# Kernel tuning notes

Measured on AMD Instinct MI355X. Metric: run time of the kernel, lower is better.

## Reference

```python
import jax, jax.numpy as jnp
import numpy as np

B, S, D = 1, 2048, 2048        # batch, max_seq_len, hidden_dim_attention
G, HPG = 4, 8                   # n_head_groups, n_heads_per_group
H = G * HPG                     # 32 total heads
DK = D // G                     # 512, KV projection width
HD = D // H                     # 64, head dim
EPS = 1e-6


def _embed_position(x, pm):
    # x: [B, S, d]; pm: [2, 1, S, D] -> uses pm[i][:, :, :d]
    d = x.shape[-1]
    _x = jnp.concatenate([-x[:, :, d // 2:], x[:, :, :d // 2]], axis=-1)
    # Faithful to source: BOTH terms use the rotated _x (source quirk).
    return _x * pm[0][:, :, :d] + _x * pm[1][:, :, :d]


def setup_inputs() -> dict:
    key = jax.random.key(0)
    k0, k1, k2, k3, k4, k5 = jax.random.split(key, 6)
    sc = 1.0 / np.sqrt(D).astype(np.float32)
    x = jax.random.normal(k0, (B, S, D), jnp.float32)
    position_matrix = jax.random.uniform(k1, (2, 1, S, D), jnp.float32)
    Wq = jax.random.normal(k2, (D, D), jnp.float32) * sc
    Wk = jax.random.normal(k3, (DK, D), jnp.float32) * sc
    Wv = jax.random.normal(k4, (DK, D), jnp.float32) * sc
    Wo = jax.random.normal(k5, (D, D), jnp.float32) * sc
    return {"x": x, "position_matrix": position_matrix,
            "Wq": Wq, "Wk": Wk, "Wv": Wv, "Wo": Wo}


def reference(x, position_matrix, Wq, Wk, Wv, Wo):
    xq = x @ Wq.T                                  # [B,S,D]
    xk = x @ Wk.T                                  # [B,S,DK]
    xv = x @ Wv.T                                  # [B,S,DK]
    xq = _embed_position(xq, position_matrix)
    xk = _embed_position(xk, position_matrix)
    # GQA expansion: replicate the DK-wide KV across G groups, split into heads.
    xk4 = jnp.broadcast_to(xk[:, :, None, :], (B, S, G, DK)).reshape(B, S, H, HD).transpose(0, 2, 1, 3)
    xv4 = jnp.broadcast_to(xv[:, :, None, :], (B, S, G, DK)).reshape(B, S, H, HD).transpose(0, 2, 1, 3)
    xq4 = xq.reshape(B, S, H, HD).transpose(0, 2, 1, 3)   # [B,H,S,HD]
    score = jnp.einsum('bhsd,bhtd->bhst', xq4, xk4) / (np.sqrt(DK) + EPS)
    # Source adds a tiny positive value (1e-10) above the diagonal, not -inf.
    mask = jnp.triu(jnp.full((S, S), 1e-10, jnp.float32), 1)
    score = score + mask
    e = jnp.exp(score.astype(jnp.float32))
    scores = (e / (jnp.sum(e, axis=-1, keepdims=True) + 1.0)).astype(xq4.dtype)
    out = jnp.einsum('bhst,bhtd->bhsd', scores, xv4)      # [B,H,S,HD]
    out = out.transpose(0, 2, 1, 3).reshape(B, S, D)
    return out @ Wo.T
```

## Files before the change

kernel.cpp:

```cpp
#include <hip/hip_runtime.h>
#include <cmath>

typedef unsigned short u16;
typedef unsigned int u32;
typedef __bf16 bf16x8 __attribute__((ext_vector_type(8)));
typedef __bf16 bf16x4 __attribute__((ext_vector_type(4)));
typedef float f32x4 __attribute__((ext_vector_type(4)));

#define S_LEN 2048
#define D_MODEL 2048
#define DK_ 512
#define PM1_OFF 4194304
#define CEXP 0.06375872f

__device__ __forceinline__ u16 f2b(float f) {
  u32 u = __float_as_uint(f);
  return (u16)((u + 0x7fffu + ((u >> 16) & 1u)) >> 16);
}

__device__ __forceinline__ void gload_lds16(const void* gp, void* lp) {
  __builtin_amdgcn_global_load_lds(
      (const __attribute__((address_space(1))) void*)gp,
      (__attribute__((address_space(3))) void*)lp, 16, 0, 0);
}

__device__ __forceinline__ void vmcnt0_barrier() {
  asm volatile("s_waitcnt vmcnt(0)" ::: "memory");
  __builtin_amdgcn_s_barrier();
}

__global__ __launch_bounds__(256) void cast_all_kernel(
    const float* __restrict__ x, const float* __restrict__ wq,
    const float* __restrict__ wk, const float* __restrict__ wv,
    const float* __restrict__ wo,
    u16* __restrict__ xb, u16* __restrict__ wqb, u16* __restrict__ wkb,
    u16* __restrict__ wvb, u16* __restrict__ wob)
{
  long i4 = (long)blockIdx.x * 256 + threadIdx.x;
  const float* src; u16* dst; long off;
  if (i4 < 1048576)       { src = x;  dst = xb;  off = i4; }
  else if (i4 < 2097152)  { src = wq; dst = wqb; off = i4 - 1048576; }
  else if (i4 < 2359296)  { src = wk; dst = wkb; off = i4 - 2097152; }
  else if (i4 < 2621440)  { src = wv; dst = wvb; off = i4 - 2359296; }
  else                    { src = wo; dst = wob; off = i4 - 2621440; }
  float4 v = *(const float4*)(src + off * 4);
  ushort4 o;
  o.x = f2b(v.x); o.y = f2b(v.y); o.z = f2b(v.z); o.w = f2b(v.w);
  *(ushort4*)(dst + off * 4) = o;
}

template<int EPI>
__global__ __launch_bounds__(256) void gemm_bt(
    const u16* __restrict__ A, const u16* __restrict__ B,
    void* __restrict__ C0, void* __restrict__ C1, void* __restrict__ C2,
    int M, int N, int K, const float* __restrict__ pm)
{
  __shared__ u16 As[2][64 * 64];
  __shared__ u16 Bs[2][128 * 64];
  const int tid = threadIdx.x;
  const int lane = tid & 63, w = tid >> 6;
  const int wr = w >> 1, wc = w & 1;
  const int l15 = lane & 15, l4 = lane >> 4;

  const int nwg = gridDim.x * gridDim.y;
  const int orig = blockIdx.y * gridDim.x + blockIdx.x;
  const int lin2 = (orig & 7) * (nwg >> 3) + (orig >> 3);
  const int m0 = (lin2 & 31) * 64;
  const int n0 = (lin2 >> 5) * 128;

  const int srow = tid >> 3;
  const int scol = ((tid & 7) ^ (srow & 7)) << 3;
  const int swz = (l15 & 7) << 3;
  const int ldsoff = (tid >> 6) << 10;
  const u16* gA = A + (size_t)(m0 + srow) * K + scol;
  const u16* gB = B + (size_t)(n0 + srow) * K + scol;

  const f32x4 z4 = {0.f, 0.f, 0.f, 0.f};
  f32x4 acc[2][4];
#pragma unroll
  for (int i = 0; i < 2; ++i)
#pragma unroll
    for (int j = 0; j < 4; ++j) acc[i][j] = z4;

  {
    char* la = (char*)As[0] + ldsoff;
    char* lb = (char*)Bs[0] + ldsoff;
#pragma unroll
    for (int i = 0; i < 2; ++i) gload_lds16(gA + (size_t)(i * 32) * K, la + i * 4096);
#pragma unroll
    for (int i = 0; i < 4; ++i) gload_lds16(gB + (size_t)(i * 32) * K, lb + i * 4096);
  }
  vmcnt0_barrier();

  const int NT = K >> 6;
  int cur = 0;
  for (int t = 0; t < NT; ++t) {
    if (t + 1 < NT) {
      const int kt = (t + 1) << 6;
      char* la = (char*)As[cur ^ 1] + ldsoff;
      char* lb = (char*)Bs[cur ^ 1] + ldsoff;
#pragma unroll
      for (int i = 0; i < 2; ++i) gload_lds16(gA + (size_t)(i * 32) * K + kt, la + i * 4096);
#pragma unroll
      for (int i = 0; i < 4; ++i) gload_lds16(gB + (size_t)(i * 32) * K + kt, lb + i * 4096);
    }
    const u16* as = As[cur];
    const u16* bs = Bs[cur];
#pragma unroll
    for (int ks = 0; ks < 2; ++ks) {
      bf16x8 a[2], b[4];
#pragma unroll
      for (int mt = 0; mt < 2; ++mt)
        a[mt] = *(const bf16x8*)(&as[(wr * 32 + mt * 16 + l15) * 64 + ((ks * 32 + l4 * 8) ^ swz)]);
#pragma unroll
      for (int nt = 0; nt < 4; ++nt)
        b[nt] = *(const bf16x8*)(&bs[(wc * 64 + nt * 16 + l15) * 64 + ((ks * 32 + l4 * 8) ^ swz)]);
#pragma unroll
      for (int mt = 0; mt < 2; ++mt)
#pragma unroll
        for (int nt = 0; nt < 4; ++nt)
          acc[mt][nt] = __builtin_amdgcn_mfma_f32_16x16x32_bf16(a[mt], b[nt], acc[mt][nt], 0, 0, 0);
    }
    vmcnt0_barrier();
    cur ^= 1;
  }

#pragma unroll
  for (int mt = 0; mt < 2; ++mt)
#pragma unroll
    for (int nt = 0; nt < 4; ++nt) {
      const int mb = m0 + wr * 32 + mt * 16 + l4 * 4;
      const int n = n0 + wc * 64 + nt * 16 + l15;
      if (EPI == 2) {
#pragma unroll
        for (int j = 0; j < 4; ++j)
          ((float*)C0)[(size_t)(mb + j) * N + n] = acc[mt][nt][j];
      } else if (n >= 2560) {
        const int c = n - 2560;
        ushort4 q;
        q.x = f2b(acc[mt][nt][0]); q.y = f2b(acc[mt][nt][1]);
        q.z = f2b(acc[mt][nt][2]); q.w = f2b(acc[mt][nt][3]);
        *(ushort4*)((u16*)C2 + (size_t)c * S_LEN + mb) = q;
      } else if (n < 2048) {
        const int jj = (n < 1024) ? (n + 1024) : (n - 1024);
#pragma unroll
        for (int j = 0; j < 4; ++j) {
          const int m = mb + j;
          const float sv = (n < 1024) ? acc[mt][nt][j] : -acc[mt][nt][j];
          const float p = pm[(size_t)m * D_MODEL + jj] +
                          pm[PM1_OFF + (size_t)m * D_MODEL + jj];
          ((u16*)C0)[(size_t)m * D_MODEL + jj] = f2b(sv * p * CEXP);
        }
      } else {
        const int nn = n - 2048;
        const int jj = (nn < 256) ? (nn + 256) : (nn - 256);
#pragma unroll
        for (int j = 0; j < 4; ++j) {
          const int m = mb + j;
          const float sv = (nn < 256) ? acc[mt][nt][j] : -acc[mt][nt][j];
          const float p = pm[(size_t)m * D_MODEL + jj] +
                          pm[PM1_OFF + (size_t)m * D_MODEL + jj];
          ((u16*)C1)[(size_t)m * DK_ + jj] = f2b(sv * p);
        }
      }
    }
}

__global__ __launch_bounds__(256) void attn_kernel(
    const u16* __restrict__ Q, const u16* __restrict__ Kx,
    const u16* __restrict__ Vt, u16* __restrict__ O)
{
  __shared__ u16 Ks[2][64 * 64];
  __shared__ u16 Vs[2][64 * 64];
  __shared__ u16 Es[4 * 32 * 64];

  const int tid = threadIdx.x;
  const int lane = tid & 63, w = tid >> 6;
  const int l15 = lane & 15, l4 = lane >> 4;

  const int orig = blockIdx.y * 16 + blockIdx.x;
  const int lin2 = (orig & 7) * 64 + (orig >> 3);
  const int h = lin2 >> 4;
  const int qb = lin2 & 15;
  const int q0 = qb * 128 + w * 32;
  const int hk = (h & 7) * 64;

  bf16x8 bq[2][2];
#pragma unroll
  for (int g = 0; g < 2; ++g)
#pragma unroll
    for (int ks = 0; ks < 2; ++ks)
      bq[g][ks] = *(const bf16x8*)(Q + (size_t)(q0 + g * 16 + l15) * D_MODEL
                                     + h * 64 + ks * 32 + l4 * 8);

  bf16x8 b1;
#pragma unroll
  for (int i = 0; i < 8; ++i) b1[i] = (__bf16)1.0f;

  const f32x4 z4 = {0.f, 0.f, 0.f, 0.f};
  f32x4 o[2][4], dsum[2];
#pragma unroll
  for (int g = 0; g < 2; ++g) {
    dsum[g] = z4;
#pragma unroll
    for (int nt = 0; nt < 4; ++nt) o[g][nt] = z4;
  }

  u16* Ew = Es + w * (32 * 64);
  const int swz = (l15 & 7) << 3;
  const int srow = tid >> 3;
  const int scol = ((tid & 7) ^ (srow & 7)) << 3;
  const int ldsoff = w << 10;
  const u16* gK = Kx + (size_t)srow * DK_ + hk + scol;
  const u16* gV = Vt + (size_t)(hk + srow) * S_LEN + scol;

  {
    char* lK = (char*)Ks[0] + ldsoff;
    char* lV = (char*)Vs[0] + ldsoff;
    gload_lds16(gK,                        lK);
    gload_lds16(gK + (size_t)32 * DK_,     lK + 4096);
    gload_lds16(gV,                        lV);
    gload_lds16(gV + (size_t)32 * S_LEN,   lV + 4096);
  }
  vmcnt0_barrier();

  int cur = 0;
  for (int t0 = 0; t0 < S_LEN; t0 += 64) {
    if (t0 + 64 < S_LEN) {
      char* lK = (char*)Ks[cur ^ 1] + ldsoff;
      char* lV = (char*)Vs[cur ^ 1] + ldsoff;
      gload_lds16(gK + (size_t)(t0 + 64) * DK_,       lK);
      gload_lds16(gK + (size_t)(t0 + 96) * DK_,       lK + 4096);
      gload_lds16(gV + t0 + 64,                       lV);
      gload_lds16(gV + t0 + 64 + (size_t)32 * S_LEN,  lV + 4096);
    }
    const u16* ks_ = Ks[cur];
    const u16* vs_ = Vs[cur];

    f32x4 sT[2][4];
#pragma unroll
    for (int g = 0; g < 2; ++g)
#pragma unroll
      for (int tf = 0; tf < 4; ++tf) sT[g][tf] = z4;
#pragma unroll
    for (int ks = 0; ks < 2; ++ks) {
      bf16x8 ak[4];
#pragma unroll
      for (int tf = 0; tf < 4; ++tf)
        ak[tf] = *(const bf16x8*)(&ks_[(tf * 16 + l15) * 64 + ((ks * 32 + l4 * 8) ^ swz)]);
      __builtin_amdgcn_s_setprio(1);
#pragma unroll
      for (int g = 0; g < 2; ++g)
#pragma unroll
        for (int tf = 0; tf < 4; ++tf)
          sT[g][tf] = __builtin_amdgcn_mfma_f32_16x16x32_bf16(ak[tf], bq[g][ks], sT[g][tf], 0, 0, 0);
      __builtin_amdgcn_s_setprio(0);
    }

#pragma unroll
    for (int g = 0; g < 2; ++g)
#pragma unroll
      for (int tf = 0; tf < 4; ++tf) {
        const float e0 = __builtin_amdgcn_exp2f(sT[g][tf][0]);
        const float e1 = __builtin_amdgcn_exp2f(sT[g][tf][1]);
        const float e2 = __builtin_amdgcn_exp2f(sT[g][tf][2]);
        const float e3 = __builtin_amdgcn_exp2f(sT[g][tf][3]);
        bf16x4 pk = {(__bf16)e0, (__bf16)e1, (__bf16)e2, (__bf16)e3};
        *(bf16x4*)(&Ew[(g * 16 + l15) * 64 + ((tf * 16 + l4 * 4) ^ swz)]) = pk;
      }

#pragma unroll
    for (int ks = 0; ks < 2; ++ks) {
      bf16x8 ae[2], bv[4];
#pragma unroll
      for (int g = 0; g < 2; ++g)
        ae[g] = *(const bf16x8*)(&Ew[(g * 16 + l15) * 64 + ((ks * 32 + l4 * 8) ^ swz)]);
#pragma unroll
      for (int nt = 0; nt < 4; ++nt)
        bv[nt] = *(const bf16x8*)(&vs_[(nt * 16 + l15) * 64 + ((ks * 32 + l4 * 8) ^ swz)]);
      __builtin_amdgcn_s_setprio(1);
#pragma unroll
      for (int g = 0; g < 2; ++g) {
#pragma unroll
        for (int nt = 0; nt < 4; ++nt)
          o[g][nt] = __builtin_amdgcn_mfma_f32_16x16x32_bf16(ae[g], bv[nt], o[g][nt], 0, 0, 0);
        dsum[g] = __builtin_amdgcn_mfma_f32_16x16x32_bf16(ae[g], b1, dsum[g], 0, 0, 0);
      }
      __builtin_amdgcn_s_setprio(0);
    }

    vmcnt0_barrier();
    cur ^= 1;
  }

#pragma unroll
  for (int g = 0; g < 2; ++g) {
    float dn[4];
#pragma unroll
    for (int j = 0; j < 4; ++j) dn[j] = dsum[g][j] + 1.0f;
#pragma unroll
    for (int nt = 0; nt < 4; ++nt)
#pragma unroll
      for (int j = 0; j < 4; ++j) {
        O[(size_t)(q0 + g * 16 + l4 * 4 + j) * D_MODEL + h * 64 + nt * 16 + l15] =
            f2b(o[g][nt][j] / dn[j]);
      }
  }
}

extern "C" void kernel_launch(void* const* d_in, const int* in_sizes, int n_in,
                              void* d_out, int out_size, void* d_ws, size_t ws_size,
                              hipStream_t stream) {
  const float* x  = (const float*)d_in[0];
  const float* pm = (const float*)d_in[1];
  const float* Wq = (const float*)d_in[2];
  const float* Wk = (const float*)d_in[3];
  const float* Wv = (const float*)d_in[4];
  const float* Wo = (const float*)d_in[5];
  float* outp = (float*)d_out;
  char* ws = (char*)d_ws;

  const size_t MB = 1024 * 1024;
  u16* xb   = (u16*)(ws + 0 * MB);
  u16* wqb  = (u16*)(ws + 8 * MB);
  u16* wkb  = (u16*)(ws + 16 * MB);
  u16* wvb  = (u16*)(ws + 18 * MB);
  u16* wob  = (u16*)(ws + 20 * MB);
  u16* qro  = (u16*)(ws + 28 * MB);
  u16* kro  = (u16*)(ws + 36 * MB);
  u16* xvt  = (u16*)(ws + 40 * MB);
  u16* attn = (u16*)(ws + 42 * MB);
  const u16* wqkv = wqb;

  cast_all_kernel<<<14336, 256, 0, stream>>>(x, Wq, Wk, Wv, Wo, xb, wqb, wkb, wvb, wob);
  gemm_bt<1><<<dim3(24, 32), 256, 0, stream>>>(xb, wqkv, (void*)qro, (void*)kro,
                                               (void*)xvt, 2048, 3072, 2048, pm);
  attn_kernel<<<dim3(16, 32), 256, 0, stream>>>(qro, kro, xvt, attn);
  gemm_bt<2><<<dim3(16, 32), 256, 0, stream>>>(attn, wob, (void*)outp, nullptr,
                                               nullptr, 2048, 2048, 2048, nullptr);
}
```

Baseline: 134.7 us.

## Split attention over two key halves and add a combine kernel

Adds a third grid dimension to the attention kernel so each block processes only half of the key/value sequence. Each block writes unnormalized bf16 partial outputs and partial denominators into workspace regions that are no longer needed. A new combine kernel sums the two partials, applies the +1 normalization and writes the attention output in row-major order. This doubles the block count to raise occupancy and latency hiding on the GPU. The cost is an extra launch, extra global traffic, and an extra bf16 rounding of the partial sums.

New measurement: 140.8 us (median of 2 runs). 1.05x slower.

```diff
diff --git a/kernel.cpp b/kernel.cpp
--- a/kernel.cpp
+++ b/kernel.cpp
@@ -12,6 +12,7 @@
 #define DK_ 512
 #define PM1_OFF 4194304
 #define CEXP 0.06375872f
+#define PSPLIT_ELEMS 4194304u
 
 __device__ __forceinline__ u16 f2b(float f) {
   u32 u = __float_as_uint(f);
@@ -168,7 +169,7 @@
 
 __global__ __launch_bounds__(256) void attn_kernel(
     const u16* __restrict__ Q, const u16* __restrict__ Kx,
-    const u16* __restrict__ Vt, u16* __restrict__ O)
+    const u16* __restrict__ Vt, u16* __restrict__ P, float* __restrict__ DN)
 {
   __shared__ u16 Ks[2][64 * 64];
   __shared__ u16 Vs[2][64 * 64];
@@ -184,6 +185,8 @@
   const int qb = lin2 & 15;
   const int q0 = qb * 128 + w * 32;
   const int hk = (h & 7) * 64;
+  const int split = blockIdx.z;
+  const int tbase = split << 10;
 
   bf16x8 bq[2][2];
 #pragma unroll
@@ -217,16 +220,17 @@
   {
     char* lK = (char*)Ks[0] + ldsoff;
     char* lV = (char*)Vs[0] + ldsoff;
-    gload_lds16(gK,                        lK);
-    gload_lds16(gK + (size_t)32 * DK_,     lK + 4096);
-    gload_lds16(gV,                        lV);
-    gload_lds16(gV + (size_t)32 * S_LEN,   lV + 4096);
+    gload_lds16(gK + (size_t)tbase * DK_,             lK);
+    gload_lds16(gK + (size_t)(tbase + 32) * DK_,      lK + 4096);
+    gload_lds16(gV + tbase,                           lV);
+    gload_lds16(gV + tbase + (size_t)32 * S_LEN,      lV + 4096);
   }
   vmcnt0_barrier();
 
   int cur = 0;
-  for (int t0 = 0; t0 < S_LEN; t0 += 64) {
-    if (t0 + 64 < S_LEN) {
+  const int tend = tbase + 1024;
+  for (int t0 = tbase; t0 < tend; t0 += 64) {
+    if (t0 + 64 < tend) {
       char* lK = (char*)Ks[cur ^ 1] + ldsoff;
       char* lV = (char*)Vs[cur ^ 1] + ldsoff;
       gload_lds16(gK + (size_t)(t0 + 64) * DK_,       lK);
@@ -293,19 +297,41 @@
     cur ^= 1;
   }
 
+  u16* Op = P + (size_t)split * PSPLIT_ELEMS;
 #pragma unroll
   for (int g = 0; g < 2; ++g) {
-    float dn[4];
-#pragma unroll
-    for (int j = 0; j < 4; ++j) dn[j] = dsum[g][j] + 1.0f;
+    const int qg = q0 + g * 16 + l4 * 4;
 #pragma unroll
     for (int nt = 0; nt < 4; ++nt)
 #pragma unroll
-      for (int j = 0; j < 4; ++j) {
-        O[(size_t)(q0 + g * 16 + l4 * 4 + j) * D_MODEL + h * 64 + nt * 16 + l15] =
-            f2b(o[g][nt][j] / dn[j]);
-      }
-  }
+      for (int j = 0; j < 4; ++j)
+        Op[((size_t)h * S_LEN + qg + j) * 64 + nt * 16 + l15] = f2b(o[g][nt][j]);
+    if (l15 == 0) {
+#pragma unroll
+      for (int j = 0; j < 4; ++j)
+        DN[(size_t)(split * 32 + h) * S_LEN + qg + j] = dsum[g][j];
+    }
+  }
+}
+
+__global__ __launch_bounds__(256) void combine_kernel(
+    const u16* __restrict__ P, const float* __restrict__ DN,
+    u16* __restrict__ A)
+{
+  const int idx = blockIdx.x * 256 + threadIdx.x;
+  const int oct = idx & 7;
+  const int q   = (idx >> 3) & 2047;
+  const int h   = idx >> 14;
+  const size_t po = ((size_t)h * S_LEN + q) * 64 + (oct << 3);
+  const bf16x8 a = *(const bf16x8*)(P + po);
+  const bf16x8 b = *(const bf16x8*)(P + PSPLIT_ELEMS + po);
+  const float r = 1.0f / (DN[(size_t)h * S_LEN + q] +
+                          DN[(size_t)(h + 32) * S_LEN + q] + 1.0f);
+  u16 out[8];
+#pragma unroll
+  for (int e = 0; e < 8; ++e)
+    out[e] = f2b(((float)a[e] + (float)b[e]) * r);
+  *(uint4*)(A + (size_t)q * D_MODEL + h * 64 + (oct << 3)) = *(uint4*)out;
 }
 
 extern "C" void kernel_launch(void* const* d_in, const int* in_sizes, int n_in,
@@ -331,11 +357,14 @@
   u16* xvt  = (u16*)(ws + 40 * MB);
   u16* attn = (u16*)(ws + 42 * MB);
   const u16* wqkv = wqb;
+  u16*   pPart = (u16*)(ws + 0 * MB);
+  float* dnb   = (float*)(ws + 16 * MB);
 
   cast_all_kernel<<<14336, 256, 0, stream>>>(x, Wq, Wk, Wv, Wo, xb, wqb, wkb, wvb, wob);
   gemm_bt<1><<<dim3(24, 32), 256, 0, stream>>>(xb, wqkv, (void*)qro, (void*)kro,
                                                (void*)xvt, 2048, 3072, 2048, pm);
-  attn_kernel<<<dim3(16, 32), 256, 0, stream>>>(qro, kro, xvt, attn);
+  attn_kernel<<<dim3(16, 32, 2), 256, 0, stream>>>(qro, kro, xvt, pPart, dnb);
+  combine_kernel<<<2048, 256, 0, stream>>>(pPart, dnb, attn);
   gemm_bt<2><<<dim3(16, 32), 256, 0, stream>>>(attn, wob, (void*)outp, nullptr,
                                                nullptr, 2048, 2048, 2048, nullptr);
 }
```
